# Performance work log

Hardware: AMD Instinct MI355X
Metric: run time of the kernel (lower is better)

## Reference

```python
import jax, jax.numpy as jnp
import numpy as np

EPS_NORM = 1e-12   # torch F.normalize eps
GN_EPS = 1e-5      # GroupNorm eps
FACTOR = 5
NUM_HEADS = 8
NEG_SLOPE = 0.01   # LeakyReLU default


def _l2norm(x, axis):
    n = jnp.sqrt(jnp.sum(x * x, axis=axis, keepdims=True))
    return x / jnp.maximum(n, EPS_NORM)


def setup_inputs() -> dict:
    key = jax.random.key(0)
    B, C, H, W, D = 2, 256, 16, 16, 16
    N = H * W * D
    sample_k = FACTOR * int(np.ceil(np.log(N)))  # 45
    ks = jax.random.split(key, 8)
    s = 0.02
    return {
        "x": jax.random.normal(ks[0], (B, C, H, W, D), jnp.float32),
        "W_qkvv": jax.random.normal(ks[1], (C, 4 * C), jnp.float32) * s,
        "W_out": jax.random.normal(ks[2], (C, C), jnp.float32) * s,
        "b_out": jnp.zeros((C,), jnp.float32),
        "W_out2": jax.random.normal(ks[3], (C, C), jnp.float32) * s,
        "b_out2": jnp.zeros((C,), jnp.float32),
        "gamma1": 0.1 * jnp.ones((C,), jnp.float32),
        "conv_w": jax.random.normal(ks[4], (C, C, 3, 3, 3), jnp.float32) * s,
        "gn_w": jnp.ones((C,), jnp.float32),
        "gn_b": jnp.zeros((C,), jnp.float32),
        "index_sample": jax.random.randint(ks[5], (N, sample_k), 0, N),
    }


def reference(x, W_qkvv, W_out, b_out, W_out2, b_out2, gamma1, conv_w, gn_w, gn_b, index_sample):
    B, C, H, Wd, D = x.shape
    N = H * Wd * D
    nh = NUM_HEADS
    dh = C // nh
    xs = x.reshape(B, C, N).transpose(0, 2, 1)                    # [B,N,C]
    qkvv = (xs @ W_qkvv).reshape(B, N, 4, nh, dh).transpose(2, 0, 3, 1, 4)  # [4,B,nh,N,dh]
    q, k, v_ca, v_sa = qkvv[0], qkvv[1], qkvv[2], qkvv[3]
    q = _l2norm(q, axis=-2)   # normalize over sequence dim (dim=-2 in torch)
    k = _l2norm(k, axis=-2)

    u = FACTOR * int(np.ceil(np.log(N)))
    # --- ProbSparse _prob_QK ---
    K_sample = k[:, :, index_sample, :]                            # [B,nh,N,sk,dh]
    QK_sample = jnp.einsum('bhle,bhlse->bhls', q, K_sample)        # [B,nh,N,sk]
    M = QK_sample.max(-1) - QK_sample.sum(-1) / N                  # sparsity measure
    _, M_top = jax.lax.top_k(M, u)                                 # [B,nh,u]
    b_idx = jnp.arange(B)[:, None, None]
    h_idx = jnp.arange(nh)[None, :, None]
    Q_red = q[b_idx, h_idx, M_top]                                 # [B,nh,u,dh]
    scores = jnp.einsum('bhud,bhld->bhul', Q_red, k)               # [B,nh,u,N]

    # --- spatial (ProbSparse) context ---
    ctx = jnp.broadcast_to(v_sa.mean(axis=-2, keepdims=True), v_sa.shape)  # [B,nh,N,dh]
    attn_sa = jax.nn.softmax(scores, axis=-1)
    upd = jnp.einsum('bhul,bhld->bhud', attn_sa, v_sa)             # [B,nh,u,dh]
    ctx = ctx.at[b_idx, h_idx, M_top].set(upd)

    # --- channel attention (on transposed q,k,v: [B,nh,dh,N]) ---
    qt = q.transpose(0, 1, 3, 2)
    kt = k.transpose(0, 1, 3, 2)
    vt = v_ca.transpose(0, 1, 3, 2)
    attn_ca = jax.nn.softmax(jnp.einsum('bhdn,bhen->bhde', qt, kt), axis=-1)  # [B,nh,dh,dh]
    x_ca = jnp.einsum('bhde,bhen->bhdn', attn_ca, vt).transpose(0, 3, 1, 2).reshape(B, N, C)
    x_sa = ctx.transpose(0, 3, 1, 2).reshape(B, N, C)              # matches source permute
    x_sa = x_sa @ W_out + b_out                                    # dead branch (source discards)
    x_ca = x_ca @ W_out2 + b_out2
    epa = x_ca  # source: x = x_SA + x_CA; x = x_CA  -> only CA branch survives

    attn = xs + gamma1 * epa                                       # [B,N,C]
    attn = attn.reshape(B, H, Wd, D, C).transpose(0, 4, 1, 2, 3)   # [B,C,H,W,D]

    # conv8: Dropout3d (eval=id) -> Conv3d(3x3x3, no bias) -> GroupNorm(1 group)
    y = jax.lax.conv_general_dilated(attn, conv_w, (1, 1, 1), [(1, 1)] * 3,
                                     dimension_numbers=('NCDHW', 'OIDHW', 'NCDHW'))
    mu = y.mean(axis=(1, 2, 3, 4), keepdims=True)
    var = y.var(axis=(1, 2, 3, 4), keepdims=True)
    y = (y - mu) / jnp.sqrt(var + GN_EPS)
    y = y * gn_w[None, :, None, None, None] + gn_b[None, :, None, None, None]
    y = y + attn
    return jnp.where(y >= 0, y, NEG_SLOPE * y)
```

## Files before the change

### kernel.cpp

```cpp
#include <hip/hip_runtime.h>
#include <hip/hip_bf16.h>
#include <stdint.h>


#define B_ 2
#define C_ 256
#define N_ 4096
#define NH 8
#define PADV 5832
#define CN  (C_*N_)
#define BCN (B_*CN)

typedef unsigned short u16;
typedef unsigned int   u32;

using frag16 = __attribute__((ext_vector_type(8))) short;
using f32x4  = __attribute__((ext_vector_type(4))) float;

__device__ __forceinline__ u16 f2bf(float f) {
    u32 u = __float_as_uint(f);
    u += 0x7fff + ((u >> 16) & 1);
    return (u16)(u >> 16);
}
__device__ __forceinline__ float bb(u16 h) { return __uint_as_float((u32)h << 16); }
__device__ __forceinline__ void gld16(const void* g, void* l) {
    __builtin_amdgcn_global_load_lds((const __attribute__((address_space(1))) u32*)g,
                                     (__attribute__((address_space(3))) u32*)l, 16, 0, 0);
}
__device__ __forceinline__ int padrow(int n) {
    int z = n >> 8, y = (n >> 4) & 15, x = n & 15;
    return (z + 1) * 324 + (y + 1) * 18 + (x + 1);
}

#define OFF_TB    0
#define OFF_SP    3145728
#define OFF_XCAB  3670016
#define OFF_PKB   0
#define OFF_Y     3145728
#define OFF_ATTB  6291456
#define OFF_ATTP  7340032
#define OFF_WT2   8833024
#define OFF_W2B   9717760
#define OFF_WQB   9750528
#define OFF_XT    9848832
#define OFF_RSQ   10897408
#define OFF_RED   10898432

__global__ __launch_bounds__(256) void k_prep(const float* __restrict__ CW, const float* __restrict__ W2,
                                              const float* __restrict__ Wq, const float* __restrict__ X,
                                              u16* __restrict__ WT2, u16* __restrict__ W2B,
                                              u16* __restrict__ Wqb, u16* __restrict__ XT,
                                              u32* __restrict__ APz, float* __restrict__ RSQ) {
    __shared__ __align__(16) float ls[6912];
    float (*ts)[33] = (float(*)[33])ls;
    float (*t64)[65] = (float(*)[65])ls;
    int blk = blockIdx.x, tid = threadIdx.x;
    if (blk < 256) {
        int co = blk;
        const float* src = CW + (size_t)co * 6912;
        for (int u = tid; u < 6912; u += 256) ls[u] = src[u];
        __syncthreads();
#pragma unroll
        for (int t = 0; t < 27; ++t)
            WT2[(((size_t)t * 256 + co) << 8) + tid] = f2bf(ls[tid * 27 + t]);
    } else if (blk < 320) {
        int bi = blk - 256; int c0 = (bi & 7) * 32, p0 = (bi >> 3) * 32;
        int tx = tid & 31, ty = tid >> 5;
#pragma unroll
        for (int i = 0; i < 4; ++i) ts[ty + i * 8][tx] = W2[(size_t)(p0 + ty + i * 8) * 256 + c0 + tx];
        __syncthreads();
#pragma unroll
        for (int i = 0; i < 4; ++i) W2B[(size_t)(c0 + ty + i * 8) * 256 + p0 + tx] = f2bf(ts[tx][ty + i * 8]);
    } else if (blk < 512) {
        int bi = blk - 320; int c0 = (bi & 7) * 32, j0 = (bi >> 3) * 32;
        int tx = tid & 31, ty = tid >> 5;
#pragma unroll
        for (int i = 0; i < 4; ++i) ts[ty + i * 8][tx] = Wq[(size_t)(c0 + ty + i * 8) * 1024 + j0 + tx];
        __syncthreads();
#pragma unroll
        for (int i = 0; i < 4; ++i) Wqb[(size_t)(j0 + ty + i * 8) * 256 + c0 + tx] = f2bf(ts[tx][ty + i * 8]);
    } else if (blk < 1024) {
        int idx = blk - 512;
        int n0 = (idx & 63) * 64, c0 = ((idx >> 6) & 3) * 64, b = idx >> 8;
        int tn = tid & 63, tc4 = tid >> 6;
        const float* Xb = X + (size_t)b * CN;
#pragma unroll
        for (int i = 0; i < 16; ++i) t64[tc4 + i * 4][tn] = Xb[(size_t)(c0 + tc4 + i * 4) * N_ + n0 + tn];
        __syncthreads();
        u16* Xo = XT + (size_t)b * N_ * C_;
#pragma unroll
        for (int i = 0; i < 16; ++i)
            Xo[(size_t)(n0 + tc4 + i * 4) * C_ + c0 + tn] = f2bf(t64[tn][tc4 + i * 4]);
    } else if (blk < 6856) {
        APz[(size_t)(blk - 1024) * 256 + tid] = 0;
    } else {
        ((float4*)RSQ)[tid] = make_float4(0.f, 0.f, 0.f, 0.f);
    }
}

__global__ __launch_bounds__(256) void k_qkv_mfma(const u16* __restrict__ Wqb, const u16* __restrict__ XT,
                                                  u16* __restrict__ Tb, float* __restrict__ RSQ) {
    __shared__ __align__(16) u16 As[2][8192], Bs[2][8192];
    int n0 = blockIdx.x * 128, j0 = blockIdx.y * 128, b = blockIdx.z;
    int tid = threadIdx.x, lane = tid & 63, w = tid >> 6;
    int wm = w & 1, wn = w >> 1, qm = lane >> 4, lm = lane & 15;
    int srow = lane >> 3;
    int sperm = (((lane & 7) ^ srow) << 3);
    const u16* aB = Wqb + ((size_t)(j0 + w * 32 + srow) << 8) + sperm;
    const u16* bB = XT + ((size_t)(b * N_ + n0 + w * 32 + srow) << 8) + sperm;
    int rdp = ((lm & 7) << 3);
    f32x4 acc[4][4] = {};
    auto stg = [&](int p, int kc) {
#pragma unroll
        for (int i = 0; i < 4; ++i) {
            gld16(aB + i * 2048 + kc * 64, &As[p][w * 2048 + i * 512]);
            gld16(bB + i * 2048 + kc * 64, &Bs[p][w * 2048 + i * 512]);
        }
    };
    stg(0, 0);
#pragma unroll
    for (int kt = 0; kt < 4; ++kt) {
        int p = kt & 1;
        __syncthreads();
        if (kt < 3) stg(p ^ 1, kt + 1);
#pragma unroll
        for (int c2 = 0; c2 < 2; ++c2) {
            frag16 af[4], bf[4];
#pragma unroll
            for (int i = 0; i < 4; ++i)
                af[i] = *(const frag16*)&As[p][(wm * 64 + i * 16 + lm) * 64 + ((((c2 * 4 + qm) << 3) ^ rdp))];
#pragma unroll
            for (int j = 0; j < 4; ++j)
                bf[j] = *(const frag16*)&Bs[p][(wn * 64 + j * 16 + lm) * 64 + ((((c2 * 4 + qm) << 3) ^ rdp))];
#pragma unroll
            for (int i = 0; i < 4; ++i)
#pragma unroll
                for (int j = 0; j < 4; ++j)
                    acc[i][j] = __builtin_amdgcn_mfma_f32_16x16x32_bf16(af[i], bf[j], acc[i][j], 0, 0, 0);
        }
    }
    u16* To = Tb + ((size_t)b * 768 + j0 + wm * 64) * N_ + n0 + wn * 64;
#pragma unroll
    for (int i = 0; i < 4; ++i)
#pragma unroll
        for (int j = 0; j < 4; ++j)
#pragma unroll
            for (int r = 0; r < 4; ++r)
                To[(size_t)(i * 16 + qm * 4 + r) * N_ + j * 16 + lm] = f2bf(acc[i][j][r]);
    if (j0 < 512) {
#pragma unroll
        for (int i = 0; i < 4; ++i)
#pragma unroll
            for (int r = 0; r < 4; ++r) {
                float s = 0.f;
#pragma unroll
                for (int j = 0; j < 4; ++j) s += acc[i][j][r] * acc[i][j][r];
                s += __shfl_xor(s, 1); s += __shfl_xor(s, 2);
                s += __shfl_xor(s, 4); s += __shfl_xor(s, 8);
                if (lm == 0)
                    atomicAdd(&RSQ[b * 512 + j0 + wm * 64 + i * 16 + qm * 4 + r], s);
            }
    }
}

__global__ __launch_bounds__(256) void k_ca_score(const u16* __restrict__ Tb, float* __restrict__ SP) {
    __shared__ __align__(16) u16 Qs[2][8192], Ks[2][8192];
    int ks = blockIdx.x, h = blockIdx.y, b = blockIdx.z;
    int tid = threadIdx.x, lane = tid & 63, w = tid >> 6;
    int wm = w & 1, wn = w >> 1, qm = lane >> 4, lm = lane & 15;
    const u16* Qb = Tb + ((size_t)b * 768 + h * 32) * N_;
    const u16* Kb = Tb + ((size_t)b * 768 + 256 + h * 32) * N_;
    int k0base = ks * 512;
    auto stg = [&](int p, int ck) {
        int k0 = k0base + ck * 256;
#pragma unroll
        for (int ri = 0; ri < 4; ++ri) {
            int row = ri * 8 + w * 2 + (lane >> 5);
            int cg = (lane & 31) ^ (row & 31);
            gld16(Qb + (size_t)row * N_ + k0 + cg * 8, &Qs[p][ri * 2048 + w * 512]);
            gld16(Kb + (size_t)row * N_ + k0 + cg * 8, &Ks[p][ri * 2048 + w * 512]);
        }
    };
    f32x4 acc = {};
    stg(0, 0);
#pragma unroll
    for (int ck = 0; ck < 2; ++ck) {
        int p = ck & 1;
        __syncthreads();
        if (ck < 1) stg(p ^ 1, ck + 1);
        int rowA = wm * 16 + lm, rowB = wn * 16 + lm;
#pragma unroll
        for (int kk = 0; kk < 8; ++kk) {
            int slotA = ((kk * 4 + qm) ^ (rowA & 31)) << 3;
            int slotB = ((kk * 4 + qm) ^ (rowB & 31)) << 3;
            frag16 af = *(const frag16*)&Qs[p][rowA * 256 + slotA];
            frag16 bf = *(const frag16*)&Ks[p][rowB * 256 + slotB];
            acc = __builtin_amdgcn_mfma_f32_16x16x32_bf16(af, bf, acc, 0, 0, 0);
        }
    }
    float* o = SP + (((size_t)(b * NH + h)) * 8 + ks) * 1024;
#pragma unroll
    for (int r = 0; r < 4; ++r)
        o[(wm * 16 + qm * 4 + r) * 32 + wn * 16 + lm] = acc[r];
}

__global__ __launch_bounds__(256) void k_ca_apply(const u16* __restrict__ Tb, const float* __restrict__ SP,
                                                  const float* __restrict__ RSQ, u16* __restrict__ XCAb) {
    int n0 = blockIdx.x * 256, h = blockIdx.y, b = blockIdx.z;
    __shared__ float raw[1024];
    __shared__ float Ae[32][32];
    __shared__ float sq[32], sk[32];
    int tid = threadIdx.x;
    const float* Sp = SP + ((size_t)(b * NH + h)) * 8192;
    for (int u = tid; u < 1024; u += 256) {
        float v = 0.f;
#pragma unroll
        for (int s = 0; s < 8; ++s) v += Sp[s * 1024 + u];
        raw[u] = v;
    }
    if (tid < 32) {
        sq[tid] = 1.0f / fmaxf(sqrtf(RSQ[b * 512 + h * 32 + tid]), 1e-12f);
        sk[tid] = 1.0f / fmaxf(sqrtf(RSQ[b * 512 + 256 + h * 32 + tid]), 1e-12f);
    }
    __syncthreads();
    if (tid < 32) {
        float iq = sq[tid];
        float sv[32]; float m = -1e30f;
#pragma unroll
        for (int e = 0; e < 32; ++e) { sv[e] = raw[tid * 32 + e] * iq * sk[e]; m = fmaxf(m, sv[e]); }
        float sm = 0.f;
#pragma unroll
        for (int e = 0; e < 32; ++e) { sv[e] = __expf(sv[e] - m); sm += sv[e]; }
        float rinv = 1.0f / sm;
#pragma unroll
        for (int e = 0; e < 32; ++e) Ae[e][tid] = sv[e] * rinv;
    }
    __syncthreads();
    int n = n0 + tid;
    const u16* V = Tb + ((size_t)b * 768 + 512 + h * 32) * N_ + n;
    float acc[32];
#pragma unroll
    for (int d = 0; d < 32; ++d) acc[d] = 0.f;
#pragma unroll
    for (int e = 0; e < 32; ++e) {
        float v = bb(V[(size_t)e * N_]);
#pragma unroll
        for (int dg = 0; dg < 8; ++dg) {
            float4 a4 = *(const float4*)&Ae[e][dg * 4];
            acc[dg * 4 + 0] += a4.x * v; acc[dg * 4 + 1] += a4.y * v;
            acc[dg * 4 + 2] += a4.z * v; acc[dg * 4 + 3] += a4.w * v;
        }
    }
    u16* o = XCAb + ((size_t)b * N_ + n) * C_ + h * 32;
#pragma unroll
    for (int dg = 0; dg < 8; ++dg) {
        ushort4 pk;
        pk.x = f2bf(acc[dg * 4 + 0]); pk.y = f2bf(acc[dg * 4 + 1]);
        pk.z = f2bf(acc[dg * 4 + 2]); pk.w = f2bf(acc[dg * 4 + 3]);
        *(ushort4*)(o + dg * 4) = pk;
    }
}

__global__ __launch_bounds__(256) void k_out2_mfma(const u16* __restrict__ W2B, const u16* __restrict__ XCAb,
                                                   const float* __restrict__ bias2, const float* __restrict__ g1,
                                                   const float* __restrict__ X, u16* __restrict__ ATTb,
                                                   u16* __restrict__ ATTp) {
    __shared__ __align__(16) u16 As[2][8192], Bs[2][8192];
    int n0 = blockIdx.x * 128, c0 = blockIdx.y * 128, b = blockIdx.z;
    int tid = threadIdx.x, lane = tid & 63, w = tid >> 6;
    int wm = w & 1, wn = w >> 1, qm = lane >> 4, lm = lane & 15;
    int srow = lane >> 3;
    int sperm = (((lane & 7) ^ srow) << 3);
    const u16* aB = W2B + ((size_t)(c0 + w * 32 + srow) << 8) + sperm;
    const u16* bB = XCAb + ((size_t)(b * N_ + n0 + w * 32 + srow) << 8) + sperm;
    int rdp = ((lm & 7) << 3);
    f32x4 acc[4][4] = {};
    auto stg = [&](int p, int kc) {
#pragma unroll
        for (int i = 0; i < 4; ++i) {
            gld16(aB + i * 2048 + kc * 64, &As[p][w * 2048 + i * 512]);
            gld16(bB + i * 2048 + kc * 64, &Bs[p][w * 2048 + i * 512]);
        }
    };
    stg(0, 0);
#pragma unroll
    for (int kt = 0; kt < 4; ++kt) {
        int p = kt & 1;
        __syncthreads();
        if (kt < 3) stg(p ^ 1, kt + 1);
#pragma unroll
        for (int c2 = 0; c2 < 2; ++c2) {
            frag16 af[4], bf[4];
#pragma unroll
            for (int i = 0; i < 4; ++i)
                af[i] = *(const frag16*)&As[p][(wm * 64 + i * 16 + lm) * 64 + ((((c2 * 4 + qm) << 3) ^ rdp))];
#pragma unroll
            for (int j = 0; j < 4; ++j)
                bf[j] = *(const frag16*)&Bs[p][(wn * 64 + j * 16 + lm) * 64 + ((((c2 * 4 + qm) << 3) ^ rdp))];
#pragma unroll
            for (int i = 0; i < 4; ++i)
#pragma unroll
                for (int j = 0; j < 4; ++j)
                    acc[i][j] = __builtin_amdgcn_mfma_f32_16x16x32_bf16(af[i], bf[j], acc[i][j], 0, 0, 0);
        }
    }
    int c_base = c0 + wm * 64, n_base = n0 + wn * 64;
    const float* xin = X + (size_t)b * CN;
    u16* Ao = ATTb + (size_t)b * CN;
    u16* Ap = ATTp + ((size_t)b * PADV << 8);
    float val[4][4][4];
#pragma unroll
    for (int i = 0; i < 4; ++i)
#pragma unroll
        for (int r = 0; r < 4; ++r) {
            int c = c_base + i * 16 + qm * 4 + r;
            float gv = g1[c], bi = bias2[c];
#pragma unroll
            for (int j = 0; j < 4; ++j) {
                int n = n_base + j * 16 + lm;
                float v = xin[(size_t)c * N_ + n] + gv * (acc[i][j][r] + bi);
                val[i][j][r] = v;
                Ao[(size_t)c * N_ + n] = f2bf(v);
            }
        }
#pragma unroll
    for (int j = 0; j < 4; ++j) {
        int n = n_base + j * 16 + lm;
        int pr = padrow(n);
#pragma unroll
        for (int i = 0; i < 4; ++i) {
            ushort4 pk;
            pk.x = f2bf(val[i][j][0]); pk.y = f2bf(val[i][j][1]);
            pk.z = f2bf(val[i][j][2]); pk.w = f2bf(val[i][j][3]);
            *(ushort4*)&Ap[((size_t)pr << 8) + c_base + i * 16 + qm * 4] = pk;
        }
    }
}

__global__ __launch_bounds__(256) void k_conv_mfma(const u16* __restrict__ WT2, const u16* __restrict__ ATTp,
                                                   u16* __restrict__ Pk) {
    __shared__ __align__(16) u16 As[2][8192], Bs[2][8192];
    int n0 = blockIdx.x * 128;
    int co0 = (blockIdx.y & 1) * 128, ks = blockIdx.y >> 1;
    int b = blockIdx.z;
    int tid = threadIdx.x, lane = tid & 63, w = tid >> 6;
    int wm = w & 1, wn = w >> 1, qm = lane >> 4, lm = lane & 15;
    int srow = lane >> 3;
    int sperm = (((lane & 7) ^ srow) << 3);
    const u16* aB = WT2 + (((size_t)ks * 9 * 256 + co0 + w * 32 + srow) << 8) + sperm;
    int prA[4];
#pragma unroll
    for (int i = 0; i < 4; ++i) prA[i] = padrow(n0 + w * 32 + i * 8 + srow) << 8;
    const u16* bB = ATTp + ((size_t)b * PADV << 8) + ((ks - 1) * 324 << 8) + sperm;
    int rdp = ((lm & 7) << 3);
    f32x4 acc[4][4] = {};
    auto stg = [&](int p, int kt) {
        int tap9 = kt >> 2, kc = kt & 3;
        int K9 = ((tap9 / 3) - 1) * 18 + (tap9 % 3 - 1);
#pragma unroll
        for (int i = 0; i < 4; ++i) {
            gld16(aB + (size_t)tap9 * 65536 + i * 2048 + kc * 64, &As[p][w * 2048 + i * 512]);
            gld16(bB + prA[i] + K9 * 256 + kc * 64,              &Bs[p][w * 2048 + i * 512]);
        }
    };
    stg(0, 0);
#pragma unroll
    for (int kt = 0; kt < 36; ++kt) {
        int p = kt & 1;
        __syncthreads();
        if (kt < 35) stg(p ^ 1, kt + 1);
#pragma unroll
        for (int c2 = 0; c2 < 2; ++c2) {
            frag16 af[4], bf[4];
#pragma unroll
            for (int i = 0; i < 4; ++i)
                af[i] = *(const frag16*)&As[p][(wm * 64 + i * 16 + lm) * 64 + ((((c2 * 4 + qm) << 3) ^ rdp))];
#pragma unroll
            for (int j = 0; j < 4; ++j)
                bf[j] = *(const frag16*)&Bs[p][(wn * 64 + j * 16 + lm) * 64 + ((((c2 * 4 + qm) << 3) ^ rdp))];
#pragma unroll
            for (int i = 0; i < 4; ++i)
#pragma unroll
                for (int j = 0; j < 4; ++j)
                    acc[i][j] = __builtin_amdgcn_mfma_f32_16x16x32_bf16(af[i], bf[j], acc[i][j], 0, 0, 0);
        }
    }
    u16* Pb = Pk + ((size_t)(ks * B_ + b) * C_ + co0 + wm * 64) * N_ + n0 + wn * 64;
#pragma unroll
    for (int i = 0; i < 4; ++i)
#pragma unroll
        for (int j = 0; j < 4; ++j)
#pragma unroll
            for (int r = 0; r < 4; ++r)
                Pb[(size_t)(i * 16 + qm * 4 + r) * N_ + j * 16 + lm] = f2bf(acc[i][j][r]);
}

__global__ __launch_bounds__(256) void k_gn_reduce(const u16* __restrict__ Pk, u16* __restrict__ Y,
                                                   float* __restrict__ RED) {
    int blk = blockIdx.x, b = blockIdx.y;
    size_t base = (size_t)b * CN + (size_t)blk * 16384;
    const u16* p0 = Pk + base;
    const u16* p1 = Pk + BCN + base;
    const u16* p2 = Pk + (size_t)2 * BCN + base;
    u16* y = Y + base;
    float s = 0.f, q = 0.f;
    for (int u = threadIdx.x * 8; u < 16384; u += 2048) {
        uint4 a = *(const uint4*)&p0[u];
        uint4 c1 = *(const uint4*)&p1[u];
        uint4 c2 = *(const uint4*)&p2[u];
        const u16 *A = (const u16*)&a, *B1 = (const u16*)&c1, *C2 = (const u16*)&c2;
        __align__(16) u16 outp[8];
#pragma unroll
        for (int i = 0; i < 8; ++i) {
            float v = bb(A[i]) + bb(B1[i]) + bb(C2[i]);
            s += v; q += v * v;
            outp[i] = f2bf(v);
        }
        *(uint4*)&y[u] = *(const uint4*)outp;
    }
#pragma unroll
    for (int off = 32; off; off >>= 1) { s += __shfl_down(s, off); q += __shfl_down(q, off); }
    __shared__ float rs_[4], rq[4];
    int lane = threadIdx.x & 63, wv = threadIdx.x >> 6;
    if (!lane) { rs_[wv] = s; rq[wv] = q; }
    __syncthreads();
    if (threadIdx.x == 0) {
        RED[((size_t)b * 64 + blk) * 2 + 0] = rs_[0] + rs_[1] + rs_[2] + rs_[3];
        RED[((size_t)b * 64 + blk) * 2 + 1] = rq[0] + rq[1] + rq[2] + rq[3];
    }
}

__global__ __launch_bounds__(256) void k_final(const u16* __restrict__ Y, const u16* __restrict__ ATTb,
                                               const float* __restrict__ RED, const float* __restrict__ gw,
                                               const float* __restrict__ gb, float* __restrict__ out) {
    int i = blockIdx.x * 256 + threadIdx.x;
    int b = i >> 20;
    int c = (i >> 12) & 255;
    __shared__ float smu[2];
    if (threadIdx.x < 64) {
        float s = RED[((size_t)b * 64 + threadIdx.x) * 2 + 0];
        float q = RED[((size_t)b * 64 + threadIdx.x) * 2 + 1];
#pragma unroll
        for (int off = 32; off; off >>= 1) { s += __shfl_down(s, off); q += __shfl_down(q, off); }
        if (threadIdx.x == 0) {
            float inv = 1.0f / (float)CN;
            float mu = s * inv, var = q * inv - mu * mu;
            smu[0] = mu; smu[1] = rsqrtf(var + 1e-5f);
        }
    }
    __syncthreads();
    float v = (bb(Y[i]) - smu[0]) * smu[1] * gw[c] + gb[c] + bb(ATTb[i]);
    out[i] = v >= 0.f ? v : 0.01f * v;
}

extern "C" void kernel_launch(void* const* d_in, const int* in_sizes, int n_in,
                              void* d_out, int out_size, void* d_ws, size_t ws_size,
                              hipStream_t stream) {
    const float* x      = (const float*)d_in[0];
    const float* Wqkvv  = (const float*)d_in[1];
    const float* W_out2 = (const float*)d_in[4];
    const float* b_out2 = (const float*)d_in[5];
    const float* gamma1 = (const float*)d_in[6];
    const float* conv_w = (const float*)d_in[7];
    const float* gn_w   = (const float*)d_in[8];
    const float* gn_b   = (const float*)d_in[9];
    float* out = (float*)d_out;
    float* ws = (float*)d_ws;

    u16*   Tb   = (u16*)(ws + OFF_TB);
    float* SP   = ws + OFF_SP;
    u16*   XCAb = (u16*)(ws + OFF_XCAB);
    u16*   Pk   = (u16*)(ws + OFF_PKB);
    u16*   Y    = (u16*)(ws + OFF_Y);
    u16*   ATTb = (u16*)(ws + OFF_ATTB);
    u16*   ATTp = (u16*)(ws + OFF_ATTP);
    u16*   WT2  = (u16*)(ws + OFF_WT2);
    u16*   W2B  = (u16*)(ws + OFF_W2B);
    u16*   Wqb  = (u16*)(ws + OFF_WQB);
    u16*   XT   = (u16*)(ws + OFF_XT);
    float* RSQ  = ws + OFF_RSQ;
    float* RED  = ws + OFF_RED;

    k_prep      <<<6857, 256, 0, stream>>>(conv_w, W_out2, Wqkvv, x, WT2, W2B, Wqb, XT, (u32*)ATTp, RSQ);
    k_qkv_mfma  <<<dim3(N_ / 128, 6, B_), 256, 0, stream>>>(Wqb, XT, Tb, RSQ);
    k_ca_score  <<<dim3(8, NH, B_), 256, 0, stream>>>(Tb, SP);
    k_ca_apply  <<<dim3(N_ / 256, NH, B_), 256, 0, stream>>>(Tb, SP, RSQ, XCAb);
    k_out2_mfma <<<dim3(N_ / 128, C_ / 128, B_), 256, 0, stream>>>(W2B, XCAb, b_out2, gamma1, x, ATTb, ATTp);
    k_conv_mfma <<<dim3(N_ / 128, 6, B_), 256, 0, stream>>>(WT2, ATTp, Pk);
    k_gn_reduce <<<dim3(64, B_), 256, 0, stream>>>(Pk, Y, RED);
    k_final     <<<(B_ * CN) / 256, 256, 0, stream>>>(Y, ATTb, RED, gn_w, gn_b, out);
}
```

Measured before the change: 173.1 us.

## Fuse GroupNorm reduce and final pass via cooperative grid sync; rebalance conv split-K

The separate GroupNorm reduction and elementwise final kernels become one cooperative kernel. It keeps the summed conv partials in registers, accumulates the statistics with atomics, grid-syncs, then normalizes and writes the output, so the bf16 Y round trip and one launch are removed. The conv split-K changes from 6 to 8 slices, each walking a contiguous 27-step range over taps and channel chunks, which gives more blocks but an extra partial buffer to sum. The out2 GEMM tile shrinks to 64 columns to launch more blocks. The cooperative grid sync adds a launch constraint, and the final pass now runs on only 128 blocks.

```diff
diff --git a/kernel.cpp b/kernel.cpp
--- a/kernel.cpp
+++ b/kernel.cpp
@@ -1,6 +1,9 @@
 #include <hip/hip_runtime.h>
 #include <hip/hip_bf16.h>
+#include <hip/hip_cooperative_groups.h>
 #include <stdint.h>
+
+namespace cg = cooperative_groups;
 
 
 #define B_ 2
@@ -36,7 +39,6 @@
 #define OFF_SP    3145728
 #define OFF_XCAB  3670016
 #define OFF_PKB   0
-#define OFF_Y     3145728
 #define OFF_ATTB  6291456
 #define OFF_ATTP  7340032
 #define OFF_WT2   8833024
@@ -50,7 +52,8 @@
                                               const float* __restrict__ Wq, const float* __restrict__ X,
                                               u16* __restrict__ WT2, u16* __restrict__ W2B,
                                               u16* __restrict__ Wqb, u16* __restrict__ XT,
-                                              u32* __restrict__ APz, float* __restrict__ RSQ) {
+                                              u32* __restrict__ APz, float* __restrict__ RSQ,
+                                              float* __restrict__ RED) {
     __shared__ __align__(16) float ls[6912];
     float (*ts)[33] = (float(*)[33])ls;
     float (*t64)[65] = (float(*)[65])ls;
@@ -95,6 +98,7 @@
         APz[(size_t)(blk - 1024) * 256 + tid] = 0;
     } else {
         ((float4*)RSQ)[tid] = make_float4(0.f, 0.f, 0.f, 0.f);
+        if (tid == 0) ((float4*)RED)[0] = make_float4(0.f, 0.f, 0.f, 0.f);
     }
 }
 
@@ -265,22 +269,23 @@
                                                    const float* __restrict__ bias2, const float* __restrict__ g1,
                                                    const float* __restrict__ X, u16* __restrict__ ATTb,
                                                    u16* __restrict__ ATTp) {
-    __shared__ __align__(16) u16 As[2][8192], Bs[2][8192];
-    int n0 = blockIdx.x * 128, c0 = blockIdx.y * 128, b = blockIdx.z;
+    __shared__ __align__(16) u16 As[2][8192], Bs[2][4096];
+    int n0 = blockIdx.x * 64, c0 = blockIdx.y * 128, b = blockIdx.z;
     int tid = threadIdx.x, lane = tid & 63, w = tid >> 6;
     int wm = w & 1, wn = w >> 1, qm = lane >> 4, lm = lane & 15;
     int srow = lane >> 3;
     int sperm = (((lane & 7) ^ srow) << 3);
     const u16* aB = W2B + ((size_t)(c0 + w * 32 + srow) << 8) + sperm;
-    const u16* bB = XCAb + ((size_t)(b * N_ + n0 + w * 32 + srow) << 8) + sperm;
+    const u16* bB = XCAb + ((size_t)(b * N_ + n0 + w * 16 + srow) << 8) + sperm;
     int rdp = ((lm & 7) << 3);
-    f32x4 acc[4][4] = {};
+    f32x4 acc[4][2] = {};
     auto stg = [&](int p, int kc) {
 #pragma unroll
-        for (int i = 0; i < 4; ++i) {
+        for (int i = 0; i < 4; ++i)
             gld16(aB + i * 2048 + kc * 64, &As[p][w * 2048 + i * 512]);
-            gld16(bB + i * 2048 + kc * 64, &Bs[p][w * 2048 + i * 512]);
-        }
+#pragma unroll
+        for (int i = 0; i < 2; ++i)
+            gld16(bB + i * 2048 + kc * 64, &Bs[p][w * 1024 + i * 512]);
     };
     stg(0, 0);
 #pragma unroll
@@ -290,25 +295,25 @@
         if (kt < 3) stg(p ^ 1, kt + 1);
 #pragma unroll
         for (int c2 = 0; c2 < 2; ++c2) {
-            frag16 af[4], bf[4];
+            frag16 af[4], bf[2];
 #pragma unroll
             for (int i = 0; i < 4; ++i)
                 af[i] = *(const frag16*)&As[p][(wm * 64 + i * 16 + lm) * 64 + ((((c2 * 4 + qm) << 3) ^ rdp))];
 #pragma unroll
-            for (int j = 0; j < 4; ++j)
-                bf[j] = *(const frag16*)&Bs[p][(wn * 64 + j * 16 + lm) * 64 + ((((c2 * 4 + qm) << 3) ^ rdp))];
+            for (int j = 0; j < 2; ++j)
+                bf[j] = *(const frag16*)&Bs[p][(wn * 32 + j * 16 + lm) * 64 + ((((c2 * 4 + qm) << 3) ^ rdp))];
 #pragma unroll
             for (int i = 0; i < 4; ++i)
 #pragma unroll
-                for (int j = 0; j < 4; ++j)
+                for (int j = 0; j < 2; ++j)
                     acc[i][j] = __builtin_amdgcn_mfma_f32_16x16x32_bf16(af[i], bf[j], acc[i][j], 0, 0, 0);
         }
     }
-    int c_base = c0 + wm * 64, n_base = n0 + wn * 64;
+    int c_base = c0 + wm * 64, n_base = n0 + wn * 32;
     const float* xin = X + (size_t)b * CN;
     u16* Ao = ATTb + (size_t)b * CN;
     u16* Ap = ATTp + ((size_t)b * PADV << 8);
-    float val[4][4][4];
+    float val[4][2][4];
 #pragma unroll
     for (int i = 0; i < 4; ++i)
 #pragma unroll
@@ -316,7 +321,7 @@
             int c = c_base + i * 16 + qm * 4 + r;
             float gv = g1[c], bi = bias2[c];
 #pragma unroll
-            for (int j = 0; j < 4; ++j) {
+            for (int j = 0; j < 2; ++j) {
                 int n = n_base + j * 16 + lm;
                 float v = xin[(size_t)c * N_ + n] + gv * (acc[i][j][r] + bi);
                 val[i][j][r] = v;
@@ -324,7 +329,7 @@
             }
         }
 #pragma unroll
-    for (int j = 0; j < 4; ++j) {
+    for (int j = 0; j < 2; ++j) {
         int n = n_base + j * 16 + lm;
         int pr = padrow(n);
 #pragma unroll
@@ -347,28 +352,31 @@
     int wm = w & 1, wn = w >> 1, qm = lane >> 4, lm = lane & 15;
     int srow = lane >> 3;
     int sperm = (((lane & 7) ^ srow) << 3);
-    const u16* aB = WT2 + (((size_t)ks * 9 * 256 + co0 + w * 32 + srow) << 8) + sperm;
+    int ks27 = ks * 27;
+    const u16* aB = WT2 + (((size_t)co0 + w * 32 + srow) << 8) + sperm;
     int prA[4];
 #pragma unroll
     for (int i = 0; i < 4; ++i) prA[i] = padrow(n0 + w * 32 + i * 8 + srow) << 8;
-    const u16* bB = ATTp + ((size_t)b * PADV << 8) + ((ks - 1) * 324 << 8) + sperm;
+    const u16* bB = ATTp + ((size_t)b * PADV << 8) + sperm;
     int rdp = ((lm & 7) << 3);
     f32x4 acc[4][4] = {};
     auto stg = [&](int p, int kt) {
-        int tap9 = kt >> 2, kc = kt & 3;
-        int K9 = ((tap9 / 3) - 1) * 18 + (tap9 % 3 - 1);
+        int g = ks27 + kt;
+        int tap = g >> 2, kc = g & 3;
+        int t9 = tap % 9;
+        int Koff = (tap / 9 - 1) * 324 + (t9 / 3 - 1) * 18 + (t9 % 3 - 1);
 #pragma unroll
         for (int i = 0; i < 4; ++i) {
-            gld16(aB + (size_t)tap9 * 65536 + i * 2048 + kc * 64, &As[p][w * 2048 + i * 512]);
-            gld16(bB + prA[i] + K9 * 256 + kc * 64,              &Bs[p][w * 2048 + i * 512]);
+            gld16(aB + (size_t)tap * 65536 + i * 2048 + kc * 64, &As[p][w * 2048 + i * 512]);
+            gld16(bB + prA[i] + Koff * 256 + kc * 64,            &Bs[p][w * 2048 + i * 512]);
         }
     };
     stg(0, 0);
 #pragma unroll
-    for (int kt = 0; kt < 36; ++kt) {
+    for (int kt = 0; kt < 27; ++kt) {
         int p = kt & 1;
         __syncthreads();
-        if (kt < 35) stg(p ^ 1, kt + 1);
+        if (kt < 26) stg(p ^ 1, kt + 1);
 #pragma unroll
         for (int c2 = 0; c2 < 2; ++c2) {
             frag16 af[4], bf[4];
@@ -395,62 +403,67 @@
                 Pb[(size_t)(i * 16 + qm * 4 + r) * N_ + j * 16 + lm] = f2bf(acc[i][j][r]);
 }
 
-__global__ __launch_bounds__(256) void k_gn_reduce(const u16* __restrict__ Pk, u16* __restrict__ Y,
-                                                   float* __restrict__ RED) {
+__global__ __launch_bounds__(256) void k_gnfinal(const u16* __restrict__ Pk, const u16* __restrict__ ATTb,
+                                                 float* __restrict__ RED, const float* __restrict__ gw,
+                                                 const float* __restrict__ gb, float* __restrict__ out) {
     int blk = blockIdx.x, b = blockIdx.y;
     size_t base = (size_t)b * CN + (size_t)blk * 16384;
     const u16* p0 = Pk + base;
-    const u16* p1 = Pk + BCN + base;
-    const u16* p2 = Pk + (size_t)2 * BCN + base;
-    u16* y = Y + base;
+    float vr[8][8];
     float s = 0.f, q = 0.f;
-    for (int u = threadIdx.x * 8; u < 16384; u += 2048) {
-        uint4 a = *(const uint4*)&p0[u];
-        uint4 c1 = *(const uint4*)&p1[u];
-        uint4 c2 = *(const uint4*)&p2[u];
-        const u16 *A = (const u16*)&a, *B1 = (const u16*)&c1, *C2 = (const u16*)&c2;
-        __align__(16) u16 outp[8];
+    int t8 = threadIdx.x * 8;
+#pragma unroll
+    for (int it = 0; it < 8; ++it) {
+        int u = t8 + it * 2048;
+        uint4 a0 = *(const uint4*)&p0[u];
+        uint4 a1 = *(const uint4*)&p0[(size_t)BCN + u];
+        uint4 a2 = *(const uint4*)&p0[(size_t)2 * BCN + u];
+        uint4 a3 = *(const uint4*)&p0[(size_t)3 * BCN + u];
+        const u16 *A = (const u16*)&a0, *B1 = (const u16*)&a1, *C2 = (const u16*)&a2, *D3 = (const u16*)&a3;
 #pragma unroll
         for (int i = 0; i < 8; ++i) {
-            float v = bb(A[i]) + bb(B1[i]) + bb(C2[i]);
-            s += v; q += v * v;
-            outp[i] = f2bf(v);
-        }
-        *(uint4*)&y[u] = *(const uint4*)outp;
+            float vv = bb(A[i]) + bb(B1[i]) + bb(C2[i]) + bb(D3[i]);
+            vr[it][i] = vv; s += vv; q += vv * vv;
+        }
     }
 #pragma unroll
     for (int off = 32; off; off >>= 1) { s += __shfl_down(s, off); q += __shfl_down(q, off); }
-    __shared__ float rs_[4], rq[4];
+    __shared__ float rs_[4], rq_[4];
+    __shared__ float smu[2];
     int lane = threadIdx.x & 63, wv = threadIdx.x >> 6;
-    if (!lane) { rs_[wv] = s; rq[wv] = q; }
+    if (!lane) { rs_[wv] = s; rq_[wv] = q; }
     __syncthreads();
     if (threadIdx.x == 0) {
-        RED[((size_t)b * 64 + blk) * 2 + 0] = rs_[0] + rs_[1] + rs_[2] + rs_[3];
-        RED[((size_t)b * 64 + blk) * 2 + 1] = rq[0] + rq[1] + rq[2] + rq[3];
-    }
-}
-
-__global__ __launch_bounds__(256) void k_final(const u16* __restrict__ Y, const u16* __restrict__ ATTb,
-                                               const float* __restrict__ RED, const float* __restrict__ gw,
-                                               const float* __restrict__ gb, float* __restrict__ out) {
-    int i = blockIdx.x * 256 + threadIdx.x;
-    int b = i >> 20;
-    int c = (i >> 12) & 255;
-    __shared__ float smu[2];
-    if (threadIdx.x < 64) {
-        float s = RED[((size_t)b * 64 + threadIdx.x) * 2 + 0];
-        float q = RED[((size_t)b * 64 + threadIdx.x) * 2 + 1];
-#pragma unroll
-        for (int off = 32; off; off >>= 1) { s += __shfl_down(s, off); q += __shfl_down(q, off); }
-        if (threadIdx.x == 0) {
-            float inv = 1.0f / (float)CN;
-            float mu = s * inv, var = q * inv - mu * mu;
-            smu[0] = mu; smu[1] = rsqrtf(var + 1e-5f);
-        }
+        atomicAdd(&RED[b * 2 + 0], rs_[0] + rs_[1] + rs_[2] + rs_[3]);
+        atomicAdd(&RED[b * 2 + 1], rq_[0] + rq_[1] + rq_[2] + rq_[3]);
+    }
+    cg::this_grid().sync();
+    if (threadIdx.x == 0) {
+        float ss = __hip_atomic_load(&RED[b * 2 + 0], __ATOMIC_RELAXED, __HIP_MEMORY_SCOPE_AGENT);
+        float qq = __hip_atomic_load(&RED[b * 2 + 1], __ATOMIC_RELAXED, __HIP_MEMORY_SCOPE_AGENT);
+        float inv = 1.0f / (float)CN;
+        float mu = ss * inv, var = qq * inv - mu * mu;
+        smu[0] = mu; smu[1] = rsqrtf(var + 1e-5f);
     }
     __syncthreads();
-    float v = (bb(Y[i]) - smu[0]) * smu[1] * gw[c] + gb[c] + bb(ATTb[i]);
-    out[i] = v >= 0.f ? v : 0.01f * v;
+    float mu = smu[0], rin = smu[1];
+#pragma unroll
+    for (int it = 0; it < 8; ++it) {
+        int u = t8 + it * 2048;
+        size_t gi = base + u;
+        int c = (int)((gi >> 12) & 255);
+        float gwc = gw[c], gbc = gb[c];
+        uint4 at = *(const uint4*)&ATTb[gi];
+        const u16* Ab = (const u16*)&at;
+        float ov[8];
+#pragma unroll
+        for (int i = 0; i < 8; ++i) {
+            float y = (vr[it][i] - mu) * rin * gwc + gbc + bb(Ab[i]);
+            ov[i] = y >= 0.f ? y : 0.01f * y;
+        }
+        *(float4*)&out[gi]     = make_float4(ov[0], ov[1], ov[2], ov[3]);
+        *(float4*)&out[gi + 4] = make_float4(ov[4], ov[5], ov[6], ov[7]);
+    }
 }
 
 extern "C" void kernel_launch(void* const* d_in, const int* in_sizes, int n_in,
@@ -471,7 +484,6 @@
     float* SP   = ws + OFF_SP;
     u16*   XCAb = (u16*)(ws + OFF_XCAB);
     u16*   Pk   = (u16*)(ws + OFF_PKB);
-    u16*   Y    = (u16*)(ws + OFF_Y);
     u16*   ATTb = (u16*)(ws + OFF_ATTB);
     u16*   ATTp = (u16*)(ws + OFF_ATTP);
     u16*   WT2  = (u16*)(ws + OFF_WT2);
@@ -481,12 +493,12 @@
     float* RSQ  = ws + OFF_RSQ;
     float* RED  = ws + OFF_RED;
 
-    k_prep      <<<6857, 256, 0, stream>>>(conv_w, W_out2, Wqkvv, x, WT2, W2B, Wqb, XT, (u32*)ATTp, RSQ);
+    k_prep      <<<6857, 256, 0, stream>>>(conv_w, W_out2, Wqkvv, x, WT2, W2B, Wqb, XT, (u32*)ATTp, RSQ, RED);
     k_qkv_mfma  <<<dim3(N_ / 128, 6, B_), 256, 0, stream>>>(Wqb, XT, Tb, RSQ);
     k_ca_score  <<<dim3(8, NH, B_), 256, 0, stream>>>(Tb, SP);
     k_ca_apply  <<<dim3(N_ / 256, NH, B_), 256, 0, stream>>>(Tb, SP, RSQ, XCAb);
-    k_out2_mfma <<<dim3(N_ / 128, C_ / 128, B_), 256, 0, stream>>>(W2B, XCAb, b_out2, gamma1, x, ATTb, ATTp);
-    k_conv_mfma <<<dim3(N_ / 128, 6, B_), 256, 0, stream>>>(WT2, ATTp, Pk);
-    k_gn_reduce <<<dim3(64, B_), 256, 0, stream>>>(Pk, Y, RED);
-    k_final     <<<(B_ * CN) / 256, 256, 0, stream>>>(Y, ATTb, RED, gn_w, gn_b, out);
-}
+    k_out2_mfma <<<dim3(N_ / 64, C_ / 128, B_), 256, 0, stream>>>(W2B, XCAb, b_out2, gamma1, x, ATTb, ATTp);
+    k_conv_mfma <<<dim3(N_ / 128, 8, B_), 256, 0, stream>>>(WT2, ATTp, Pk);
+    void* gf_args[] = {(void*)&Pk, (void*)&ATTb, (void*)&RED, (void*)&gn_w, (void*)&gn_b, (void*)&out};
+    hipLaunchCooperativeKernel((const void*)k_gnfinal, dim3(64, B_), dim3(256), gf_args, 0, stream);
+}
```

Measured after the change: 213.2 us. +23.2%, slower.
